# Kernel tuning notes

Measured on AMD Instinct MI355X. Metric: run time of the kernel, lower is better.

The kernel has to match this reference:

```python
import jax, jax.numpy as jnp
import numpy as np

B, S, H = 128, 1024, 256
NEG = 1e9

def setup_inputs() -> dict:
    key = jax.random.key(0)
    ks = jax.random.split(key, 11)
    sc = 0.05
    return {
        'ref': jax.random.normal(ks[0], (B, S, H), jnp.float32),
        'query': jax.random.normal(ks[1], (B, H), jnp.float32),
        'mask': jax.random.randint(ks[2], (B, S), 0, 2, jnp.int32),
        'wg': jax.random.normal(ks[3], (H, H), jnp.float32) * sc,
        'bg': jax.random.normal(ks[4], (H,), jnp.float32) * sc,
        'wqg': jax.random.normal(ks[5], (H, H), jnp.float32) * sc,
        'vg': jax.random.normal(ks[6], (H,), jnp.float32) * sc,
        'wp': jax.random.normal(ks[7], (H, H), jnp.float32) * sc,
        'bp': jax.random.normal(ks[8], (H,), jnp.float32) * sc,
        'wqp': jax.random.normal(ks[9], (H, H), jnp.float32) * sc,
        'vp': jax.random.normal(ks[10], (H,), jnp.float32) * sc,
    }

def reference(ref, query, mask, wg, bg, wqg, vg, wp, bp, wqp, vp):
    # Bahdanau additive pointer attention with glimpse, per PointerDecoder.pointer_net
    maskf = mask.astype(ref.dtype)
    # glimpse attention
    enc_g = jnp.einsum('bsd,hd->bsh', ref, wg) + bg            # conv1d kernel=1
    q_g = jnp.einsum('bd,hd->bh', query, wqg)                   # w_q_g (no bias)
    scores_g = jnp.einsum('bsh,h->bs', jnp.tanh(enc_g + q_g[:, None, :]), vg)
    att_g = jax.nn.softmax(scores_g - maskf * NEG, axis=-1)     # [B,S]
    glimpse = jnp.einsum('bs,bsd->bd', att_g, ref) + query      # [B,H]
    # pointer scores
    enc_p = jnp.einsum('bsd,hd->bsh', ref, wp) + bp
    q_p = jnp.einsum('bd,hd->bh', glimpse, wqp)
    scores_p = jnp.einsum('bsh,h->bs', jnp.tanh(enc_p + q_p[:, None, :]), vp)
    masked_scores = scores_p - maskf * NEG                      # [B,S]
    return masked_scores
```

## Files before the change

kernel.cpp:

```cpp
#include <hip/hip_runtime.h>

#define Bb 128
#define Ss 1024
#define Hh 256
#define NEGF 1e9f

typedef short bf16x8 __attribute__((ext_vector_type(8)));
typedef float f32x4 __attribute__((ext_vector_type(4)));

__device__ __forceinline__ short f2bf(float f) {
    union { float f; unsigned u; } c; c.f = f;
    return (short)((c.u + 0x8000u) >> 16);
}

__device__ __forceinline__ float bfhi2f(unsigned u) {
    union { unsigned u; float f; } c; c.u = u & 0xFFFF0000u; return c.f;
}
__device__ __forceinline__ float bflo2f(unsigned u) {
    union { unsigned u; float f; } c; c.u = u << 16; return c.f;
}

__device__ __forceinline__ bf16x8 ld_bf8_f32(const float* p) {
    const float4* p4 = (const float4*)p;
    float4 a = p4[0], b = p4[1];
    bf16x8 r;
    r[0] = f2bf(a.x); r[1] = f2bf(a.y); r[2] = f2bf(a.z); r[3] = f2bf(a.w);
    r[4] = f2bf(b.x); r[5] = f2bf(b.y); r[6] = f2bf(b.z); r[7] = f2bf(b.w);
    return r;
}

__device__ __forceinline__ float fast_tanh(float x) {
    float cl = fminf(fmaxf(x, -10.f), 10.f);
    float e = __expf(2.f * cl);
    return (e - 1.f) * __builtin_amdgcn_rcpf(e + 1.f);
}

__device__ __forceinline__ void stage16(const short* g, short* l) {
    __builtin_amdgcn_global_load_lds((const __attribute__((address_space(1))) void*)g,
                                     (__attribute__((address_space(3))) void*)l, 16, 0, 0);
}

__global__ __launch_bounds__(256) void prep_kernel(const float* __restrict__ wg,
                                                   const float* __restrict__ wp,
                                                   const float* __restrict__ query,
                                                   const float* __restrict__ wqg,
                                                   const float* __restrict__ bg,
                                                   short* __restrict__ wgb,
                                                   short* __restrict__ wpb,
                                                   float* __restrict__ qbias_g) {
    int blk = blockIdx.x, t = threadIdx.x;
    if (blk < 256) {
        int i = blk * 256 + t;
        wgb[i] = f2bf(wg[i]);
        wpb[i] = f2bf(wp[i]);
    } else {
        int b = blk - 256;
        const float4* qr = (const float4*)(query + b * Hh);
        const float4* wr = (const float4*)(wqg + t * Hh);
        float acc = 0.f;
#pragma unroll 8
        for (int i = 0; i < Hh / 4; ++i) {
            float4 q4 = qr[i], w4 = wr[i];
            acc += q4.x * w4.x + q4.y * w4.y + q4.z * w4.z + q4.w * w4.w;
        }
        qbias_g[b * Hh + t] = acc + bg[t];
    }
}

template <int MASKED, int LOADF32>
__global__ __launch_bounds__(256) void scores_mfma(const float* __restrict__ reff,
                                                   const short* __restrict__ refb_in,
                                                   short* __restrict__ refb_out,
                                                   const short* __restrict__ Wbf,
                                                   const float* __restrict__ qbias,
                                                   const float* __restrict__ vvec,
                                                   const int* __restrict__ mask,
                                                   float* __restrict__ out) {
    __shared__ short Wlds[2][8192];
    const int b = blockIdx.x;
    const int s0 = blockIdx.y * 128;
    const int t = threadIdx.x;
    const int wave = t >> 6;
    const int lane = t & 63;
    const int nl = lane & 15;
    const int quad = lane >> 4;
    const int rowbase = s0 + wave * 32;

    const int soff0 = (t & 15) * Hh + (t >> 6) * 32 + ((t >> 4) & 3) * 8;
    const int soff1 = soff0 + 128;
    const int dbase0 = wave * 512;
    const int dbase1 = 2048 + wave * 512;

    bf16x8 afrag[2][8];
#pragma unroll
    for (int rt = 0; rt < 2; ++rt) {
        const size_t rowoff = ((size_t)b * Ss + rowbase + rt * 16 + nl) * Hh;
        if (LOADF32) {
            const float* rp = reff + rowoff;
#pragma unroll
            for (int kb = 0; kb < 8; ++kb)
                afrag[rt][kb] = ld_bf8_f32(rp + kb * 32 + quad * 8);
            short* dst = refb_out + rowoff;
#pragma unroll
            for (int kb = 0; kb < 8; ++kb)
                *(bf16x8*)(dst + kb * 32 + quad * 8) = afrag[rt][kb];
        } else {
            const short* rp = refb_in + rowoff;
#pragma unroll
            for (int kb = 0; kb < 8; ++kb)
                afrag[rt][kb] = *(const bf16x8*)(rp + kb * 32 + quad * 8);
        }
    }

    stage16(Wbf + soff0, &Wlds[0][dbase0]);
    stage16(Wbf + soff1, &Wlds[0][dbase1]);
    stage16(Wbf + 16 * Hh + soff0, &Wlds[0][4096 + dbase0]);
    stage16(Wbf + 16 * Hh + soff1, &Wlds[0][4096 + dbase1]);
    __syncthreads();

    float sc[2][4] = {{0.f, 0.f, 0.f, 0.f}, {0.f, 0.f, 0.f, 0.f}};

    for (int nc2 = 0; nc2 < 8; ++nc2) {
        const int cur = nc2 & 1;
        if (nc2 < 7) {
            const short* g = Wbf + (size_t)(nc2 + 1) * 32 * Hh;
            stage16(g + soff0, &Wlds[1 - cur][dbase0]);
            stage16(g + soff1, &Wlds[1 - cur][dbase1]);
            stage16(g + 16 * Hh + soff0, &Wlds[1 - cur][4096 + dbase0]);
            stage16(g + 16 * Hh + soff1, &Wlds[1 - cur][4096 + dbase1]);
        }
#pragma unroll
        for (int h = 0; h < 2; ++h) {
            const int n = nc2 * 32 + h * 16 + nl;
            const float qb = qbias[b * Hh + n];
            const float vv = vvec[n];
            bf16x8 bfrag[8];
#pragma unroll
            for (int kb = 0; kb < 8; ++kb)
                bfrag[kb] = *(const bf16x8*)&Wlds[cur][h * 4096 + kb * 512 + lane * 8];
#pragma unroll
            for (int rt = 0; rt < 2; ++rt) {
                f32x4 c = {0.f, 0.f, 0.f, 0.f};
#pragma unroll
                for (int kb = 0; kb < 8; ++kb)
                    c = __builtin_amdgcn_mfma_f32_16x16x32_bf16(afrag[rt][kb], bfrag[kb], c, 0, 0, 0);
#pragma unroll
                for (int r = 0; r < 4; ++r)
                    sc[rt][r] += fast_tanh(c[r] + qb) * vv;
            }
        }
        __syncthreads();
    }

#pragma unroll
    for (int rt = 0; rt < 2; ++rt)
#pragma unroll
        for (int r = 0; r < 4; ++r) {
            float v = sc[rt][r];
            v += __shfl_xor(v, 1, 64);
            v += __shfl_xor(v, 2, 64);
            v += __shfl_xor(v, 4, 64);
            v += __shfl_xor(v, 8, 64);
            sc[rt][r] = v;
        }

    if (nl == 0) {
#pragma unroll
        for (int rt = 0; rt < 2; ++rt)
#pragma unroll
            for (int r = 0; r < 4; ++r) {
                int m = rowbase + rt * 16 + quad * 4 + r;
                float v = sc[rt][r];
                if (MASKED) v -= (float)mask[b * Ss + m] * NEGF;
                out[(size_t)b * Ss + m] = v;
            }
    }
}

__global__ __launch_bounds__(1024) void softmax_kernel(const float* __restrict__ scores,
                                                       const int* __restrict__ mask,
                                                       float* __restrict__ att) {
    int b = blockIdx.x, t = threadIdx.x;
    __shared__ float red[16];
    int idx = b * Ss + t;
    float x = scores[idx] - (float)mask[idx] * NEGF;

    float m = x;
#pragma unroll
    for (int o = 1; o < 64; o <<= 1) m = fmaxf(m, __shfl_xor(m, o, 64));
    if ((t & 63) == 0) red[t >> 6] = m;
    __syncthreads();
    float M = red[0];
#pragma unroll
    for (int j = 1; j < 16; ++j) M = fmaxf(M, red[j]);
    __syncthreads();

    float e = __expf(x - M);
    float s = e;
#pragma unroll
    for (int o = 1; o < 64; o <<= 1) s += __shfl_xor(s, o, 64);
    if ((t & 63) == 0) red[t >> 6] = s;
    __syncthreads();
    float S = 0.f;
#pragma unroll
    for (int j = 0; j < 16; ++j) S += red[j];

    att[idx] = e * __builtin_amdgcn_rcpf(S);
}

__global__ __launch_bounds__(256) void glimpse_part(const unsigned* __restrict__ refb,
                                                    const float* __restrict__ att,
                                                    float* __restrict__ gpart) {
    int b = blockIdx.x, q = blockIdx.y, t = threadIdx.x;
    const int c = t & 31;
    const int rg = t >> 5;
    __shared__ float part[8][Hh];
    const unsigned* base = refb + ((size_t)(b * Ss + q * 128)) * (Hh / 2);
    const float* ap = att + b * Ss + q * 128;

    float acc[8] = {0.f, 0.f, 0.f, 0.f, 0.f, 0.f, 0.f, 0.f};
#pragma unroll 4
    for (int it = 0; it < 16; ++it) {
        int row = it * 8 + rg;
        float a = ap[row];
        uint4 v = *(const uint4*)(base + (size_t)row * (Hh / 2) + c * 4);
        acc[0] += a * bflo2f(v.x); acc[1] += a * bfhi2f(v.x);
        acc[2] += a * bflo2f(v.y); acc[3] += a * bfhi2f(v.y);
        acc[4] += a * bflo2f(v.z); acc[5] += a * bfhi2f(v.z);
        acc[6] += a * bflo2f(v.w); acc[7] += a * bfhi2f(v.w);
    }
#pragma unroll
    for (int j = 0; j < 8; ++j) part[rg][c * 8 + j] = acc[j];
    __syncthreads();
    float s = 0.f;
#pragma unroll
    for (int g = 0; g < 8; ++g) s += part[g][t];
    gpart[(size_t)(b * 8 + q) * Hh + t] = s;
}

__global__ __launch_bounds__(256) void qbias_p_kernel(const float* __restrict__ gpart,
                                                      const float* __restrict__ query,
                                                      const float* __restrict__ wqp,
                                                      const float* __restrict__ bp,
                                                      float* __restrict__ out) {
    int b = blockIdx.x, t = threadIdx.x;
    __shared__ __align__(16) float gl[Hh];
    float g = query[b * Hh + t];
#pragma unroll
    for (int q = 0; q < 8; ++q) g += gpart[(b * 8 + q) * Hh + t];
    gl[t] = g;
    __syncthreads();
    const float4* wr = (const float4*)(wqp + t * Hh);
    const float4* gp = (const float4*)gl;
    float acc = 0.f;
#pragma unroll 8
    for (int i = 0; i < Hh / 4; ++i) {
        float4 w4 = wr[i];
        float4 g4 = gp[i];
        acc += w4.x * g4.x + w4.y * g4.y + w4.z * g4.z + w4.w * g4.w;
    }
    out[b * Hh + t] = acc + bp[t];
}

extern "C" void kernel_launch(void* const* d_in, const int* in_sizes, int n_in,
                              void* d_out, int out_size, void* d_ws, size_t ws_size,
                              hipStream_t stream) {
    const float* ref   = (const float*)d_in[0];
    const float* query = (const float*)d_in[1];
    const int*   mask  = (const int*)d_in[2];
    const float* wg    = (const float*)d_in[3];
    const float* bg    = (const float*)d_in[4];
    const float* wqg   = (const float*)d_in[5];
    const float* vg    = (const float*)d_in[6];
    const float* wp    = (const float*)d_in[7];
    const float* bp    = (const float*)d_in[8];
    const float* wqp   = (const float*)d_in[9];
    const float* vp    = (const float*)d_in[10];
    float* out = (float*)d_out;

    char* ws = (char*)d_ws;
    short* ref_bf   = (short*)(ws + 0);
    size_t off = (size_t)Bb * Ss * Hh * 2;
    short* wg_bf    = (short*)(ws + off);               off += 131072;
    short* wp_bf    = (short*)(ws + off);               off += 131072;
    float* qbias_g  = (float*)(ws + off);               off += 131072;
    float* qbias_p  = (float*)(ws + off);               off += 131072;
    float* scores_g = (float*)(ws + off);               off += 524288;
    float* att      = (float*)(ws + off);               off += 524288;
    float* gpart    = (float*)(ws + off);

    prep_kernel<<<384, 256, 0, stream>>>(wg, wp, query, wqg, bg, wg_bf, wp_bf, qbias_g);
    scores_mfma<0, 1><<<dim3(Bb, Ss / 128), 256, 0, stream>>>(
        ref, nullptr, ref_bf, wg_bf, qbias_g, vg, nullptr, scores_g);
    softmax_kernel<<<Bb, Ss, 0, stream>>>(scores_g, mask, att);
    glimpse_part<<<dim3(Bb, 8), 256, 0, stream>>>((const unsigned*)ref_bf, att, gpart);
    qbias_p_kernel<<<Bb, Hh, 0, stream>>>(gpart, query, wqp, bp, qbias_p);
    scores_mfma<1, 0><<<dim3(Bb, Ss / 128), 256, 0, stream>>>(
        nullptr, ref_bf, nullptr, wp_bf, qbias_p, vp, mask, out);
}
```

Measured before the change: 298.3 us.

## Halve rows per block in scores kernel and simplify tanh formula

The MFMA scoring kernel now gives each wave one 16-row tile instead of two, launching twice as many blocks with half the LDS W buffer and half the A-fragment registers. This should raise occupancy and memory-level parallelism. In exchange, each W chunk is reused across fewer rows, so LDS staging traffic per row doubles and there are more loop iterations and barriers. The W prefetch is also issued before the A-fragment loads so the two overlap, and tanh is rewritten as 1 - 2/(e+1) to save a subtraction and a multiply.

Result: slower. 318.7 us (+6.8%).

```diff
diff --git a/kernel.cpp b/kernel.cpp
--- a/kernel.cpp
+++ b/kernel.cpp
@@ -32,7 +32,7 @@
 __device__ __forceinline__ float fast_tanh(float x) {
     float cl = fminf(fmaxf(x, -10.f), 10.f);
     float e = __expf(2.f * cl);
-    return (e - 1.f) * __builtin_amdgcn_rcpf(e + 1.f);
+    return __builtin_fmaf(-2.f, __builtin_amdgcn_rcpf(e + 1.f), 1.f);
 }
 
 __device__ __forceinline__ void stage16(const short* g, short* l) {
@@ -76,104 +76,89 @@
                                                    const float* __restrict__ vvec,
                                                    const int* __restrict__ mask,
                                                    float* __restrict__ out) {
-    __shared__ short Wlds[2][8192];
+    __shared__ short Wlds[2][4096];
     const int b = blockIdx.x;
-    const int s0 = blockIdx.y * 128;
+    const int s0 = blockIdx.y * 64;
     const int t = threadIdx.x;
     const int wave = t >> 6;
     const int lane = t & 63;
     const int nl = lane & 15;
     const int quad = lane >> 4;
-    const int rowbase = s0 + wave * 32;
+    const int rowbase = s0 + wave * 16;
 
     const int soff0 = (t & 15) * Hh + (t >> 6) * 32 + ((t >> 4) & 3) * 8;
     const int soff1 = soff0 + 128;
     const int dbase0 = wave * 512;
     const int dbase1 = 2048 + wave * 512;
 
-    bf16x8 afrag[2][8];
-#pragma unroll
-    for (int rt = 0; rt < 2; ++rt) {
-        const size_t rowoff = ((size_t)b * Ss + rowbase + rt * 16 + nl) * Hh;
+    stage16(Wbf + soff0, &Wlds[0][dbase0]);
+    stage16(Wbf + soff1, &Wlds[0][dbase1]);
+
+    bf16x8 afrag[8];
+    {
+        const size_t rowoff = ((size_t)b * Ss + rowbase + nl) * Hh;
         if (LOADF32) {
             const float* rp = reff + rowoff;
 #pragma unroll
             for (int kb = 0; kb < 8; ++kb)
-                afrag[rt][kb] = ld_bf8_f32(rp + kb * 32 + quad * 8);
+                afrag[kb] = ld_bf8_f32(rp + kb * 32 + quad * 8);
             short* dst = refb_out + rowoff;
 #pragma unroll
             for (int kb = 0; kb < 8; ++kb)
-                *(bf16x8*)(dst + kb * 32 + quad * 8) = afrag[rt][kb];
+                *(bf16x8*)(dst + kb * 32 + quad * 8) = afrag[kb];
         } else {
             const short* rp = refb_in + rowoff;
 #pragma unroll
             for (int kb = 0; kb < 8; ++kb)
-                afrag[rt][kb] = *(const bf16x8*)(rp + kb * 32 + quad * 8);
-        }
-    }
-
-    stage16(Wbf + soff0, &Wlds[0][dbase0]);
-    stage16(Wbf + soff1, &Wlds[0][dbase1]);
-    stage16(Wbf + 16 * Hh + soff0, &Wlds[0][4096 + dbase0]);
-    stage16(Wbf + 16 * Hh + soff1, &Wlds[0][4096 + dbase1]);
-    __syncthreads();
-
-    float sc[2][4] = {{0.f, 0.f, 0.f, 0.f}, {0.f, 0.f, 0.f, 0.f}};
-
-    for (int nc2 = 0; nc2 < 8; ++nc2) {
-        const int cur = nc2 & 1;
-        if (nc2 < 7) {
-            const short* g = Wbf + (size_t)(nc2 + 1) * 32 * Hh;
+                afrag[kb] = *(const bf16x8*)(rp + kb * 32 + quad * 8);
+        }
+    }
+    __syncthreads();
+
+    float sc[4] = {0.f, 0.f, 0.f, 0.f};
+
+    for (int nc = 0; nc < 16; ++nc) {
+        const int cur = nc & 1;
+        if (nc < 15) {
+            const short* g = Wbf + (size_t)(nc + 1) * 16 * Hh;
             stage16(g + soff0, &Wlds[1 - cur][dbase0]);
             stage16(g + soff1, &Wlds[1 - cur][dbase1]);
-            stage16(g + 16 * Hh + soff0, &Wlds[1 - cur][4096 + dbase0]);
-            stage16(g + 16 * Hh + soff1, &Wlds[1 - cur][4096 + dbase1]);
-        }
-#pragma unroll
-        for (int h = 0; h < 2; ++h) {
-            const int n = nc2 * 32 + h * 16 + nl;
-            const float qb = qbias[b * Hh + n];
-            const float vv = vvec[n];
-            bf16x8 bfrag[8];
-#pragma unroll
-            for (int kb = 0; kb < 8; ++kb)
-                bfrag[kb] = *(const bf16x8*)&Wlds[cur][h * 4096 + kb * 512 + lane * 8];
-#pragma unroll
-            for (int rt = 0; rt < 2; ++rt) {
-                f32x4 c = {0.f, 0.f, 0.f, 0.f};
-#pragma unroll
-                for (int kb = 0; kb < 8; ++kb)
-                    c = __builtin_amdgcn_mfma_f32_16x16x32_bf16(afrag[rt][kb], bfrag[kb], c, 0, 0, 0);
-#pragma unroll
-                for (int r = 0; r < 4; ++r)
-                    sc[rt][r] += fast_tanh(c[r] + qb) * vv;
-            }
-        }
+        }
+        const int n = nc * 16 + nl;
+        const float qb = qbias[b * Hh + n];
+        const float vv = vvec[n];
+        bf16x8 bfrag[8];
+#pragma unroll
+        for (int kb = 0; kb < 8; ++kb)
+            bfrag[kb] = *(const bf16x8*)&Wlds[cur][kb * 512 + lane * 8];
+        f32x4 c = {0.f, 0.f, 0.f, 0.f};
+#pragma unroll
+        for (int kb = 0; kb < 8; ++kb)
+            c = __builtin_amdgcn_mfma_f32_16x16x32_bf16(afrag[kb], bfrag[kb], c, 0, 0, 0);
+#pragma unroll
+        for (int r = 0; r < 4; ++r)
+            sc[r] += fast_tanh(c[r] + qb) * vv;
         __syncthreads();
     }
 
 #pragma unroll
-    for (int rt = 0; rt < 2; ++rt)
+    for (int r = 0; r < 4; ++r) {
+        float v = sc[r];
+        v += __shfl_xor(v, 1, 64);
+        v += __shfl_xor(v, 2, 64);
+        v += __shfl_xor(v, 4, 64);
+        v += __shfl_xor(v, 8, 64);
+        sc[r] = v;
+    }
+
+    if (nl == 0) {
 #pragma unroll
         for (int r = 0; r < 4; ++r) {
-            float v = sc[rt][r];
-            v += __shfl_xor(v, 1, 64);
-            v += __shfl_xor(v, 2, 64);
-            v += __shfl_xor(v, 4, 64);
-            v += __shfl_xor(v, 8, 64);
-            sc[rt][r] = v;
-        }
-
-    if (nl == 0) {
-#pragma unroll
-        for (int rt = 0; rt < 2; ++rt)
-#pragma unroll
-            for (int r = 0; r < 4; ++r) {
-                int m = rowbase + rt * 16 + quad * 4 + r;
-                float v = sc[rt][r];
-                if (MASKED) v -= (float)mask[b * Ss + m] * NEGF;
-                out[(size_t)b * Ss + m] = v;
-            }
+            int m = rowbase + quad * 4 + r;
+            float v = sc[r];
+            if (MASKED) v -= (float)mask[b * Ss + m] * NEGF;
+            out[(size_t)b * Ss + m] = v;
+        }
     }
 }
 
@@ -290,11 +275,11 @@
     float* gpart    = (float*)(ws + off);
 
     prep_kernel<<<384, 256, 0, stream>>>(wg, wp, query, wqg, bg, wg_bf, wp_bf, qbias_g);
-    scores_mfma<0, 1><<<dim3(Bb, Ss / 128), 256, 0, stream>>>(
+    scores_mfma<0, 1><<<dim3(Bb, Ss / 64), 256, 0, stream>>>(
         ref, nullptr, ref_bf, wg_bf, qbias_g, vg, nullptr, scores_g);
     softmax_kernel<<<Bb, Ss, 0, stream>>>(scores_g, mask, att);
     glimpse_part<<<dim3(Bb, 8), 256, 0, stream>>>((const unsigned*)ref_bf, att, gpart);
     qbias_p_kernel<<<Bb, Hh, 0, stream>>>(gpart, query, wqp, bp, qbias_p);
-    scores_mfma<1, 0><<<dim3(Bb, Ss / 128), 256, 0, stream>>>(
+    scores_mfma<1, 0><<<dim3(Bb, Ss / 64), 256, 0, stream>>>(
         nullptr, ref_bf, nullptr, wp_bf, qbias_p, vp, mask, out);
 }
```
